# Kernel tuning notes

Measured on AMD Instinct MI355X. Metric: run time of the kernel, lower is better.

Reference implementation:

```python
import jax, jax.numpy as jnp
import numpy as np

B, S, D, H = 8, 1024, 768, 12
HD = D // H  # head_dim = 64


def setup_inputs() -> dict:
    key = jax.random.key(0)
    ks = jax.random.split(key, 9)
    s = 0.02
    return {
        "hidden_states": jax.random.normal(ks[0], (B, S, D), dtype=jnp.float32),
        "Wq": jax.random.normal(ks[1], (D, D), dtype=jnp.float32) * s,
        "bq": jnp.zeros((D,), dtype=jnp.float32),
        "Wk": jax.random.normal(ks[2], (D, D), dtype=jnp.float32) * s,
        "bk": jnp.zeros((D,), dtype=jnp.float32),
        "Wv": jax.random.normal(ks[3], (D, D), dtype=jnp.float32) * s,
        "bv": jnp.zeros((D,), dtype=jnp.float32),
        "Wo": jax.random.normal(ks[4], (D, D), dtype=jnp.float32) * s,
        "bo": jnp.zeros((D,), dtype=jnp.float32),
    }


def reference(hidden_states, Wq, bq, Wk, bk, Wv, bv, Wo, bo):
    b, s, d = hidden_states.shape
    scale = 1.0 / jnp.sqrt(jnp.asarray(HD, dtype=hidden_states.dtype))
    # projections (weights stored as [in, out])
    q = hidden_states @ Wq + bq
    k = hidden_states @ Wk + bk
    v = hidden_states @ Wv + bv
    # [B, H, S, HD]
    q = q.reshape(b, s, H, HD).transpose(0, 2, 1, 3)
    k = k.reshape(b, s, H, HD).transpose(0, 2, 1, 3)
    v = v.reshape(b, s, H, HD).transpose(0, 2, 1, 3)
    # explicit O(S^2) attention, matching the original unfused math
    attn = jnp.einsum("bhqd,bhkd->bhqk", q, k) * scale
    attn = jax.nn.softmax(attn, axis=-1)
    out = jnp.einsum("bhqk,bhkd->bhqd", attn, v)
    out = out.transpose(0, 2, 1, 3).reshape(b, s, d)
    return out @ Wo + bo
```

## Files before the change

kernel.cpp:

```cpp
#include <hip/hip_runtime.h>
#include <stdint.h>

#define DEV __device__ __forceinline__

typedef __attribute__((ext_vector_type(8))) short bf16x8;
typedef __attribute__((ext_vector_type(4))) float f32x4;

#define MFMA16(a,b,c) __builtin_amdgcn_mfma_f32_16x16x32_bf16((a),(b),(c),0,0,0)

DEV unsigned short f2bf(float x){
  union { float f; unsigned u; } v; v.f = x;
  unsigned r = v.u + 0x7fffu + ((v.u >> 16) & 1u);
  return (unsigned short)(r >> 16);
}
DEV unsigned pack2(float a, float b){
  return (unsigned)f2bf(a) | ((unsigned)f2bf(b) << 16);
}
DEV bf16x8 mk_bf16x8(unsigned w0, unsigned w1, unsigned w2, unsigned w3){
  union { uint4 u; bf16x8 v; } cv;
  cv.u = make_uint4(w0, w1, w2, w3);
  return cv.v;
}

__global__ void cast_x_kernel(const float* __restrict__ x, uint4* __restrict__ out){
  int i = blockIdx.x * 256 + threadIdx.x;
  const float4* p = (const float4*)x + (size_t)i * 2;
  float4 a = p[0], b = p[1];
  out[i] = make_uint4(pack2(a.x,a.y), pack2(a.z,a.w), pack2(b.x,b.y), pack2(b.z,b.w));
}

__global__ void trans_w_kernel(const float* __restrict__ W0, const float* __restrict__ W1,
                               const float* __restrict__ W2, const float* __restrict__ W3,
                               unsigned short* __restrict__ T0, unsigned short* __restrict__ T1,
                               unsigned short* __restrict__ T2, unsigned short* __restrict__ T3){
  const float* W; unsigned short* T;
  switch (blockIdx.z) {
    case 0:  W = W0; T = T0; break;
    case 1:  W = W1; T = T1; break;
    case 2:  W = W2; T = T2; break;
    default: W = W3; T = T3; break;
  }
  __shared__ float tile[32][33];
  const int i0 = blockIdx.y * 32, o0 = blockIdx.x * 32;
  const int t = threadIdx.x;
  const int ir = t >> 3, oc = (t & 7) * 4;
  float4 v = *(const float4*)(W + (size_t)(i0 + ir) * 768 + o0 + oc);
  tile[ir][oc+0] = v.x; tile[ir][oc+1] = v.y; tile[ir][oc+2] = v.z; tile[ir][oc+3] = v.w;
  __syncthreads();
  const int orow = t >> 3, ic = (t & 7) * 4;
  uint2 w;
  w.x = pack2(tile[ic+0][orow], tile[ic+1][orow]);
  w.y = pack2(tile[ic+2][orow], tile[ic+3][orow]);
  *(uint2*)(T + (size_t)(o0 + orow) * 768 + i0 + ic) = w;
}

__launch_bounds__(256, 3)
__global__ void gemm_qkv(const unsigned short* __restrict__ Wcat,
                         const unsigned short* __restrict__ X16,
                         const float* __restrict__ bq, const float* __restrict__ bk,
                         const float* __restrict__ bv,
                         unsigned short* __restrict__ Qb, unsigned short* __restrict__ Kb,
                         unsigned short* __restrict__ VTb)
{
  __shared__ __align__(16) unsigned char lds[4][8192];
  const int lane = threadIdx.x & 63, wid = threadIdx.x >> 6;
  const int m0 = blockIdx.x * 128, n0 = blockIdx.y * 128;
  const int wm = wid >> 1, wn = wid & 1;

  f32x4 acc[4][4] = {};

  for (int t = 0; t < 24; ++t) {
    const int buf = t & 1;
    const int k0 = t * 32;
    #pragma unroll
    for (int i = 0; i < 2; ++i) {
      const int c   = i * 256 + wid * 64 + lane;
      const int row = ((c >> 6) << 4) + (c & 15);
      const int kk  = ((c >> 4) & 3) * 8;
      const unsigned short* sa = Wcat + (size_t)(m0 + row) * 768 + k0 + kk;
      const unsigned short* sb = X16  + (size_t)(n0 + row) * 768 + k0 + kk;
      __builtin_amdgcn_global_load_lds(
          (const __attribute__((address_space(1))) void*)sa,
          (__attribute__((address_space(3))) void*)&lds[buf][(i * 256 + wid * 64) * 16],
          16, 0, 0);
      __builtin_amdgcn_global_load_lds(
          (const __attribute__((address_space(1))) void*)sb,
          (__attribute__((address_space(3))) void*)&lds[2 + buf][(i * 256 + wid * 64) * 16],
          16, 0, 0);
    }
    __syncthreads();

    bf16x8 afr[4], bfr[4];
    #pragma unroll
    for (int mb = 0; mb < 4; ++mb)
      afr[mb] = *(const bf16x8*)&lds[buf][((wm * 4 + mb) * 64 + lane) * 16];
    #pragma unroll
    for (int nb = 0; nb < 4; ++nb)
      bfr[nb] = *(const bf16x8*)&lds[2 + buf][((wn * 4 + nb) * 64 + lane) * 16];
    #pragma unroll
    for (int mb = 0; mb < 4; ++mb)
      #pragma unroll
      for (int nb = 0; nb < 4; ++nb)
        acc[mb][nb] = MFMA16(afr[mb], bfr[nb], acc[mb][nb]);
  }

  const int l15 = lane & 15, lg = lane >> 4;
  const int sel = m0 / 768;
  const int mbase = m0 - sel * 768;
  #pragma unroll
  for (int mb = 0; mb < 4; ++mb) {
    #pragma unroll
    for (int nb = 0; nb < 4; ++nb) {
      const int rowl = wm * 64 + mb * 16 + lg * 4;
      const int coll = wn * 64 + nb * 16 + l15;
      f32x4 a = acc[mb][nb];
      const int chan = mbase + rowl;
      const int sg   = n0 + coll;
      const int b = sg >> 10, s = sg & 1023, h = chan >> 6, hd = chan & 63;
      if (sel != 2) {
        float4 bi = *(const float4*)((sel == 0 ? bq : bk) + chan);
        uint2 w;
        w.x = pack2(a[0] + bi.x, a[1] + bi.y);
        w.y = pack2(a[2] + bi.z, a[3] + bi.w);
        unsigned short* o = (sel == 0 ? Qb : Kb);
        *(uint2*)(o + ((size_t)(b * 12 + h) * 1024 + s) * 64 + hd) = w;
      } else {
        float4 bi = *(const float4*)(bv + chan);
        size_t base = ((size_t)(b * 12 + h) * 64 + hd) * 1024 + s;
        VTb[base       ] = f2bf(a[0] + bi.x);
        VTb[base + 1024] = f2bf(a[1] + bi.y);
        VTb[base + 2048] = f2bf(a[2] + bi.z);
        VTb[base + 3072] = f2bf(a[3] + bi.w);
      }
    }
  }
}

__launch_bounds__(256, 3)
__global__ void gemm_out(const unsigned short* __restrict__ matA,
                         const unsigned short* __restrict__ matB,
                         float* __restrict__ outp,
                         const float* __restrict__ bias)
{
  __shared__ __align__(16) unsigned char lds[4][8192];
  const int lane = threadIdx.x & 63, wid = threadIdx.x >> 6;
  const int m0 = blockIdx.x * 128, n0 = blockIdx.y * 128;
  const int wm = wid >> 1, wn = wid & 1;

  f32x4 acc[4][4] = {};

  for (int t = 0; t < 24; ++t) {
    const int buf = t & 1;
    const int k0 = t * 32;
    #pragma unroll
    for (int i = 0; i < 2; ++i) {
      const int c   = i * 256 + wid * 64 + lane;
      const int row = ((c >> 6) << 4) + (c & 15);
      const int kk  = ((c >> 4) & 3) * 8;
      const unsigned short* sa = matA + (size_t)(m0 + row) * 768 + k0 + kk;
      const unsigned short* sb = matB + (size_t)(n0 + row) * 768 + k0 + kk;
      __builtin_amdgcn_global_load_lds(
          (const __attribute__((address_space(1))) void*)sa,
          (__attribute__((address_space(3))) void*)&lds[buf][(i * 256 + wid * 64) * 16],
          16, 0, 0);
      __builtin_amdgcn_global_load_lds(
          (const __attribute__((address_space(1))) void*)sb,
          (__attribute__((address_space(3))) void*)&lds[2 + buf][(i * 256 + wid * 64) * 16],
          16, 0, 0);
    }
    __syncthreads();

    bf16x8 afr[4], bfr[4];
    #pragma unroll
    for (int mb = 0; mb < 4; ++mb)
      afr[mb] = *(const bf16x8*)&lds[buf][((wm * 4 + mb) * 64 + lane) * 16];
    #pragma unroll
    for (int nb = 0; nb < 4; ++nb)
      bfr[nb] = *(const bf16x8*)&lds[2 + buf][((wn * 4 + nb) * 64 + lane) * 16];
    #pragma unroll
    for (int mb = 0; mb < 4; ++mb)
      #pragma unroll
      for (int nb = 0; nb < 4; ++nb)
        acc[mb][nb] = MFMA16(afr[mb], bfr[nb], acc[mb][nb]);
  }

  const int l15 = lane & 15, lg = lane >> 4;
  #pragma unroll
  for (int mb = 0; mb < 4; ++mb) {
    #pragma unroll
    for (int nb = 0; nb < 4; ++nb) {
      const int rowl = wm * 64 + mb * 16 + lg * 4;
      const int coll = wn * 64 + nb * 16 + l15;
      f32x4 a = acc[mb][nb];
      int chan = m0 + rowl, sg = n0 + coll;
      float4 bi = *(const float4*)(bias + chan);
      float4 o = make_float4(a[0] + bi.x, a[1] + bi.y, a[2] + bi.z, a[3] + bi.w);
      *(float4*)(outp + (size_t)sg * 768 + chan) = o;
    }
  }
}

__launch_bounds__(256, 4)
__global__ void attn_kernel(const unsigned short* __restrict__ Q,
                            const unsigned short* __restrict__ K,
                            const unsigned short* __restrict__ VT,
                            unsigned short* __restrict__ AO)
{
  __shared__ __align__(16) unsigned char kbuf[8192];
  __shared__ __align__(16) unsigned char vbuf[8192];
  const int lane = threadIdx.x & 63, wid = threadIdx.x >> 6;
  const int l15 = lane & 15, lg = lane >> 4;
  const int bh = blockIdx.x;
  const int q0 = blockIdx.y * 128 + wid * 32;
  const unsigned short* Qp = Q  + (size_t)bh * 65536;
  const unsigned short* Kp = K  + (size_t)bh * 65536;
  const unsigned short* Vp = VT + (size_t)bh * 65536;

  bf16x8 qf[2][2];
  #pragma unroll
  for (int f = 0; f < 2; ++f)
    #pragma unroll
    for (int kc = 0; kc < 2; ++kc)
      qf[f][kc] = *(const bf16x8*)(Qp + (size_t)(q0 + f * 16 + l15) * 64 + kc * 32 + lg * 8);

  f32x4 acco[2][4] = {};
  float lsum[2] = {0.f, 0.f};

  const int src0 = l15 + ((lg & 1) << 5);
  const int src1 = src0 + 16;
  const bool hi = (lg & 2) != 0;

  for (int t = 0; t < 16; ++t) {
    const int kv0 = t * 64;
    #pragma unroll
    for (int i = 0; i < 2; ++i) {
      const int g = wid * 2 + i;
      const unsigned short* sk = Kp + (size_t)(kv0 + (g >> 1) * 16 + l15) * 64 + (g & 1) * 32 + lg * 8;
      __builtin_amdgcn_global_load_lds(
          (const __attribute__((address_space(1))) void*)sk,
          (__attribute__((address_space(3))) void*)&kbuf[g * 1024], 16, 0, 0);
      const unsigned short* sv = Vp + (size_t)((g >> 1) * 16 + l15) * 1024 + kv0 + (g & 1) * 32 + lg * 8;
      __builtin_amdgcn_global_load_lds(
          (const __attribute__((address_space(1))) void*)sv,
          (__attribute__((address_space(3))) void*)&vbuf[g * 1024], 16, 0, 0);
    }
    __syncthreads();

    f32x4 sc[2][4] = {};
    #pragma unroll
    for (int mb = 0; mb < 4; ++mb) {
      #pragma unroll
      for (int kc = 0; kc < 2; ++kc) {
        bf16x8 kf = *(const bf16x8*)&kbuf[((mb * 2 + kc) * 64 + lane) * 16];
        sc[0][mb] = MFMA16(kf, qf[0][kc], sc[0][mb]);
        sc[1][mb] = MFMA16(kf, qf[1][kc], sc[1][mb]);
      }
    }
    unsigned p01[2][4], p23[2][4];
    #pragma unroll
    for (int f = 0; f < 2; ++f) {
      float sum = 0.f;
      #pragma unroll
      for (int mb = 0; mb < 4; ++mb) {
        float e0 = __expf(sc[f][mb][0] * 0.125f);
        float e1 = __expf(sc[f][mb][1] * 0.125f);
        float e2 = __expf(sc[f][mb][2] * 0.125f);
        float e3 = __expf(sc[f][mb][3] * 0.125f);
        sum += (e0 + e1) + (e2 + e3);
        p01[f][mb] = pack2(e0, e1);
        p23[f][mb] = pack2(e2, e3);
      }
      sum += __shfl_xor(sum, 16);
      sum += __shfl_xor(sum, 32);
      lsum[f] += sum;
    }
    bf16x8 pf[2][2];
    #pragma unroll
    for (int f = 0; f < 2; ++f) {
      #pragma unroll
      for (int c = 0; c < 2; ++c) {
        unsigned a0 = __shfl(p01[f][2*c], src0), b0 = __shfl(p01[f][2*c+1], src0);
        unsigned a1 = __shfl(p23[f][2*c], src0), b1 = __shfl(p23[f][2*c+1], src0);
        unsigned a2 = __shfl(p01[f][2*c], src1), b2 = __shfl(p01[f][2*c+1], src1);
        unsigned a3 = __shfl(p23[f][2*c], src1), b3 = __shfl(p23[f][2*c+1], src1);
        pf[f][c] = mk_bf16x8(hi ? b0 : a0, hi ? b1 : a1, hi ? b2 : a2, hi ? b3 : a3);
      }
    }
    #pragma unroll
    for (int hb = 0; hb < 4; ++hb) {
      #pragma unroll
      for (int c = 0; c < 2; ++c) {
        bf16x8 vf = *(const bf16x8*)&vbuf[((hb * 2 + c) * 64 + lane) * 16];
        acco[0][hb] = MFMA16(vf, pf[0][c], acco[0][hb]);
        acco[1][hb] = MFMA16(vf, pf[1][c], acco[1][hb]);
      }
    }
    __syncthreads();
  }

  const int b = bh / 12, h = bh % 12;
  #pragma unroll
  for (int f = 0; f < 2; ++f) {
    const float rl = 1.0f / lsum[f];
    const int s = q0 + f * 16 + l15;
    const size_t base = ((size_t)(b * 1024 + s)) * 768 + h * 64;
    #pragma unroll
    for (int hb = 0; hb < 4; ++hb) {
      uint2 w;
      w.x = pack2(acco[f][hb][0] * rl, acco[f][hb][1] * rl);
      w.y = pack2(acco[f][hb][2] * rl, acco[f][hb][3] * rl);
      *(uint2*)(AO + base + hb * 16 + lg * 4) = w;
    }
  }
}

extern "C" void kernel_launch(void* const* d_in, const int* in_sizes, int n_in,
                              void* d_out, int out_size, void* d_ws, size_t ws_size,
                              hipStream_t stream)
{
  const float* hs = (const float*)d_in[0];
  const float* Wq = (const float*)d_in[1];
  const float* bq = (const float*)d_in[2];
  const float* Wk = (const float*)d_in[3];
  const float* bk = (const float*)d_in[4];
  const float* Wv = (const float*)d_in[5];
  const float* bv = (const float*)d_in[6];
  const float* Wo = (const float*)d_in[7];
  const float* bo = (const float*)d_in[8];

  const size_t SZ_X = (size_t)8192 * 768 * 2;
  const size_t SZ_W = (size_t)768 * 768 * 2;
  const size_t NEED = SZ_X * 5 + SZ_W * 4;
  if (ws_size < NEED) return;

  char* ws = (char*)d_ws;
  unsigned short* X16 = (unsigned short*)ws;
  unsigned short* Wqt = (unsigned short*)(ws + SZ_X);
  unsigned short* Wkt = Wqt + 768 * 768;
  unsigned short* Wvt = Wkt + 768 * 768;
  unsigned short* Wot = Wvt + 768 * 768;
  unsigned short* Qb  = (unsigned short*)(ws + SZ_X + 4 * SZ_W);
  unsigned short* Kb  = Qb  + (size_t)8192 * 768;
  unsigned short* VTb = Kb  + (size_t)8192 * 768;
  unsigned short* AOb = VTb + (size_t)8192 * 768;

  cast_x_kernel<<<dim3(3072), dim3(256), 0, stream>>>(hs, (uint4*)X16);
  trans_w_kernel<<<dim3(24, 24, 4), dim3(256), 0, stream>>>(Wq, Wk, Wv, Wo, Wqt, Wkt, Wvt, Wot);

  gemm_qkv<<<dim3(18, 64), dim3(256), 0, stream>>>(Wqt, X16, bq, bk, bv, Qb, Kb, VTb);

  attn_kernel<<<dim3(96, 8), dim3(256), 0, stream>>>(Qb, Kb, VTb, AOb);

  gemm_out<<<dim3(6, 64), dim3(256), 0, stream>>>(Wot, AOb, (float*)d_out, bo);
}
```

Baseline: 173.1 us.

## Remap GEMM blocks across XCDs and halve output GEMM M-tile

New measurement: 174.5 us. About the same (+0.8%).

```diff
diff --git a/kernel.cpp b/kernel.cpp
--- a/kernel.cpp
+++ b/kernel.cpp
@@ -54,7 +54,7 @@
   *(uint2*)(T + (size_t)(o0 + orow) * 768 + i0 + ic) = w;
 }
 
-__launch_bounds__(256, 3)
+__launch_bounds__(256, 4)
 __global__ void gemm_qkv(const unsigned short* __restrict__ Wcat,
                          const unsigned short* __restrict__ X16,
                          const float* __restrict__ bq, const float* __restrict__ bk,
@@ -64,7 +64,10 @@
 {
   __shared__ __align__(16) unsigned char lds[4][8192];
   const int lane = threadIdx.x & 63, wid = threadIdx.x >> 6;
-  const int m0 = blockIdx.x * 128, n0 = blockIdx.y * 128;
+  const int lin = blockIdx.x;
+  const int nid = (lin & 7) * 144 + (lin >> 3);
+  const int m0 = (nid % 18) * 128;
+  const int n0 = (nid / 18) * 128;
   const int wm = wid >> 1, wn = wid & 1;
 
   f32x4 acc[4][4] = {};
@@ -142,43 +145,50 @@
                          float* __restrict__ outp,
                          const float* __restrict__ bias)
 {
-  __shared__ __align__(16) unsigned char lds[4][8192];
+  __shared__ __align__(16) unsigned char ldsA[2][4096];
+  __shared__ __align__(16) unsigned char ldsB[2][8192];
   const int lane = threadIdx.x & 63, wid = threadIdx.x >> 6;
-  const int m0 = blockIdx.x * 128, n0 = blockIdx.y * 128;
+  const int lin = blockIdx.x;
+  const int nid = (lin & 7) * 96 + (lin >> 3);
+  const int m0 = (nid % 12) * 64;
+  const int n0 = (nid / 12) * 128;
   const int wm = wid >> 1, wn = wid & 1;
 
-  f32x4 acc[4][4] = {};
+  f32x4 acc[2][4] = {};
 
   for (int t = 0; t < 24; ++t) {
     const int buf = t & 1;
     const int k0 = t * 32;
+    {
+      const int c   = wid * 64 + lane;
+      const int row = ((c >> 6) << 4) + (c & 15);
+      const int kk  = ((c >> 4) & 3) * 8;
+      const unsigned short* sa = matA + (size_t)(m0 + row) * 768 + k0 + kk;
+      __builtin_amdgcn_global_load_lds(
+          (const __attribute__((address_space(1))) void*)sa,
+          (__attribute__((address_space(3))) void*)&ldsA[buf][c * 16], 16, 0, 0);
+    }
     #pragma unroll
     for (int i = 0; i < 2; ++i) {
       const int c   = i * 256 + wid * 64 + lane;
       const int row = ((c >> 6) << 4) + (c & 15);
       const int kk  = ((c >> 4) & 3) * 8;
-      const unsigned short* sa = matA + (size_t)(m0 + row) * 768 + k0 + kk;
       const unsigned short* sb = matB + (size_t)(n0 + row) * 768 + k0 + kk;
       __builtin_amdgcn_global_load_lds(
-          (const __attribute__((address_space(1))) void*)sa,
-          (__attribute__((address_space(3))) void*)&lds[buf][(i * 256 + wid * 64) * 16],
-          16, 0, 0);
-      __builtin_amdgcn_global_load_lds(
           (const __attribute__((address_space(1))) void*)sb,
-          (__attribute__((address_space(3))) void*)&lds[2 + buf][(i * 256 + wid * 64) * 16],
-          16, 0, 0);
+          (__attribute__((address_space(3))) void*)&ldsB[buf][c * 16], 16, 0, 0);
     }
     __syncthreads();
 
-    bf16x8 afr[4], bfr[4];
-    #pragma unroll
-    for (int mb = 0; mb < 4; ++mb)
-      afr[mb] = *(const bf16x8*)&lds[buf][((wm * 4 + mb) * 64 + lane) * 16];
+    bf16x8 afr[2], bfr[4];
+    #pragma unroll
+    for (int mb = 0; mb < 2; ++mb)
+      afr[mb] = *(const bf16x8*)&ldsA[buf][((wm * 2 + mb) * 64 + lane) * 16];
     #pragma unroll
     for (int nb = 0; nb < 4; ++nb)
-      bfr[nb] = *(const bf16x8*)&lds[2 + buf][((wn * 4 + nb) * 64 + lane) * 16];
-    #pragma unroll
-    for (int mb = 0; mb < 4; ++mb)
+      bfr[nb] = *(const bf16x8*)&ldsB[buf][((wn * 4 + nb) * 64 + lane) * 16];
+    #pragma unroll
+    for (int mb = 0; mb < 2; ++mb)
       #pragma unroll
       for (int nb = 0; nb < 4; ++nb)
         acc[mb][nb] = MFMA16(afr[mb], bfr[nb], acc[mb][nb]);
@@ -186,10 +196,10 @@
 
   const int l15 = lane & 15, lg = lane >> 4;
   #pragma unroll
-  for (int mb = 0; mb < 4; ++mb) {
+  for (int mb = 0; mb < 2; ++mb) {
     #pragma unroll
     for (int nb = 0; nb < 4; ++nb) {
-      const int rowl = wm * 64 + mb * 16 + lg * 4;
+      const int rowl = wm * 32 + mb * 16 + lg * 4;
       const int coll = wn * 64 + nb * 16 + l15;
       f32x4 a = acc[mb][nb];
       int chan = m0 + rowl, sg = n0 + coll;
@@ -347,9 +357,9 @@
   cast_x_kernel<<<dim3(3072), dim3(256), 0, stream>>>(hs, (uint4*)X16);
   trans_w_kernel<<<dim3(24, 24, 4), dim3(256), 0, stream>>>(Wq, Wk, Wv, Wo, Wqt, Wkt, Wvt, Wot);
 
-  gemm_qkv<<<dim3(18, 64), dim3(256), 0, stream>>>(Wqt, X16, bq, bk, bv, Qb, Kb, VTb);
+  gemm_qkv<<<dim3(1152), dim3(256), 0, stream>>>(Wqt, X16, bq, bk, bv, Qb, Kb, VTb);
 
   attn_kernel<<<dim3(96, 8), dim3(256), 0, stream>>>(Qb, Kb, VTb, AOb);
 
-  gemm_out<<<dim3(6, 64), dim3(256), 0, stream>>>(Wot, AOb, (float*)d_out, bo);
-}
+  gemm_out<<<dim3(768), dim3(256), 0, stream>>>(Wot, AOb, (float*)d_out, bo);
+}
```
